# Kernel optimization log

Measured on AMD Instinct MI355X. Metric: run time of the kernel, lower is better.

Reference implementation:

```python
import jax, jax.numpy as jnp
from jax import lax
import numpy as np

N_PATTS, D_PATTS, L_PATTS = 64, 16, 64
L_OUT = L_PATTS  # module sets l_out = l_patts in both branches
RHO = 0.1
W = RHO ** (1.0 / L_PATTS)  # per-step decay weight
BIG = 1e30  # stands in for +inf at DP boundaries (avoids inf*0 nans)


def _dtw_matrix(x, patts, w):
    """Weighted-DTW DP matrix.
    x: (B, d, T), patts: (P, d, L) -> D: (B, P, L, T)
    D[i,j] = dist[i,j] + w * min(D[i-1,j], D[i,j-1], D[i-1,j-1]),
    with out-of-range predecessors = +inf and D[0,0] = dist[0,0].
    dist is the euclidean distance between x[:, :, j] and patts[:, :, i].
    """
    B, d, T = x.shape
    P, _, L = patts.shape
    x2 = jnp.sum(x * x, axis=1)              # (B, T)
    p2 = jnp.sum(patts * patts, axis=1)      # (P, L)
    xp = jnp.einsum('bdt,pdl->btpl', x, patts)  # (B, T, P, L)
    sq = x2[:, :, None, None] + p2[None, None, :, :] - 2.0 * xp
    dist = jnp.sqrt(jnp.maximum(sq, 1e-12))  # (B, T, P, L)
    dist_t = jnp.transpose(dist, (1, 0, 2, 3))  # (T, B, P, L) scan over time

    def col_step(prev_col, d_col):
        # prev_col = D[:, j-1] of shape (B, P, L); d_col = dist column (B, P, L)
        shifted = jnp.concatenate(
            [jnp.full_like(prev_col[..., :1], BIG), prev_col[..., :-1]], axis=-1)
        c = jnp.minimum(prev_col, shifted)  # min(D[i,j-1], D[i-1,j-1]) per i

        def cell(d_prev, inp):
            dist_i, c_i = inp              # each (B, P)
            m = jnp.minimum(d_prev, c_i)   # min over the 3 predecessors
            val = dist_i + jnp.where(m >= BIG * 0.5, 0.0, w * m)
            return val, val

        init = jnp.full(prev_col.shape[:2], BIG, prev_col.dtype)  # D[-1, j]
        _, col = lax.scan(
            cell, init,
            (jnp.moveaxis(d_col, -1, 0), jnp.moveaxis(c, -1, 0)))  # over i
        col = jnp.moveaxis(col, 0, -1)  # (B, P, L)
        return col, col

    init_col = jnp.full((B, P, L), BIG, dist.dtype)  # D[:, -1] = inf
    _, cols = lax.scan(col_step, init_col, dist_t)   # (T, B, P, L)
    return jnp.transpose(cols, (1, 2, 3, 0))         # (B, P, L, T)


def setup_inputs() -> dict:
    key = jax.random.key(0)
    kx, kp = jax.random.split(key)
    x = jax.random.normal(kx, (16, D_PATTS, 1024), dtype=jnp.float32)
    patts = jax.random.normal(kp, (N_PATTS, D_PATTS, L_PATTS), dtype=jnp.float32)
    return {"x": x, "patts": patts}


def reference(x, patts):
    D = _dtw_matrix(x, patts, W)          # (B, P, L, T)
    return D[:, :, :, -L_OUT:]            # last l_out time steps
```

## Files before the change

kernel.cpp:

```cpp
#include <hip/hip_runtime.h>
#include <math.h>

typedef _Float16 half8 __attribute__((ext_vector_type(8)));
typedef _Float16 h2 __attribute__((ext_vector_type(2)));
typedef float    f32x4 __attribute__((ext_vector_type(4)));
typedef unsigned int u32;
typedef unsigned long long u64;
typedef unsigned short u16;

#define BIGV 1e30f
#define RSTR 36

__device__ __forceinline__ u32 dpp_shr1(u32 oldv, u32 src) {
  return (u32)__builtin_amdgcn_update_dpp((int)oldv, (int)src, 0x138, 0xF, 0xF, false);
}
__device__ __forceinline__ float cvtlo(u32 v) {
  union { u16 u; _Float16 h; } c; c.u = (u16)v; return (float)c.h;
}
__device__ __forceinline__ u16 f2h(float f) {
  union { _Float16 h; u16 u; } c; c.h = (_Float16)f; return c.u;
}
__device__ __forceinline__ u32 pkrtz(float a, float b) {
  auto v = __builtin_amdgcn_cvt_pkrtz(a, b);
  union { decltype(v) h; u32 u; } c; c.h = v; return c.u;
}
__device__ __forceinline__ u32 funnel16(u32 hi, u32 lo, u32 sh) {
  return (u32)(((((u64)hi) << 32) | (u64)lo) >> sh);
}
__device__ __forceinline__ h2 as_h2(u32 u) { union { u32 u; h2 h; } x; x.u = u; return x.h; }

__global__ __launch_bounds__(256) void dtw_pc4(
    const float* __restrict__ x,
    const float* __restrict__ patts,
    float* __restrict__ out,
    float w) {
  __shared__ uint4 xsq[2050];
  __shared__ uint2 ring2[2 * 64 * RSTR];
  __shared__ u16   x2h16[1024];

  const int tid = threadIdx.x, lane = tid & 63, wv = tid >> 6;
  const int b = blockIdx.x >> 5, pg = blockIdx.x & 31;
  const int role = wv >> 1, pr = wv & 1;
  const int p = pg * 2 + pr;
  const int le = lane & 15, kq = lane >> 4;

  {
    const float* xb = x + b * (16 * 1024);
    u16* xh = (u16*)xsq;
    for (int idx = tid; idx < 16384; idx += 256) {
      int d = idx >> 10, t = idx & 1023;
      xh[t * 16 + d] = f2h(xb[idx]);
    }
    if (tid == 0) { xsq[2048] = make_uint4(0,0,0,0); xsq[2049] = make_uint4(0,0,0,0); }
    __syncthreads();
    for (int t = tid; t < 1024; t += 256) {
      uint4 a0 = xsq[2 * t], a1 = xsq[2 * t + 1];
      float s2 = __builtin_amdgcn_fdot2(as_h2(a0.x), as_h2(a0.x), 0.f, false);
      s2 = __builtin_amdgcn_fdot2(as_h2(a0.y), as_h2(a0.y), s2, false);
      s2 = __builtin_amdgcn_fdot2(as_h2(a0.z), as_h2(a0.z), s2, false);
      s2 = __builtin_amdgcn_fdot2(as_h2(a0.w), as_h2(a0.w), s2, false);
      s2 = __builtin_amdgcn_fdot2(as_h2(a1.x), as_h2(a1.x), s2, false);
      s2 = __builtin_amdgcn_fdot2(as_h2(a1.y), as_h2(a1.y), s2, false);
      s2 = __builtin_amdgcn_fdot2(as_h2(a1.z), as_h2(a1.z), s2, false);
      s2 = __builtin_amdgcn_fdot2(as_h2(a1.w), as_h2(a1.w), s2, false);
      x2h16[t] = f2h(s2);
    }
  }
  __syncthreads();

  if (role == 0) {
    half8 bf[4];
    {
      const float* pp = patts + p * (16 * 64);
#pragma unroll
      for (int nb = 0; nb < 4; ++nb) {
        float pv[8]; float part = 0.f;
#pragma unroll
        for (int j = 0; j < 8; ++j) {
          float f = (kq < 2) ? pp[(8 * kq + j) * 64 + nb * 16 + le] : 0.f;
          pv[j] = f; part = fmaf(f, f, part);
        }
        part += __shfl_xor(part, 16, 64);
        part += __shfl_xor(part, 32, 64);
        u32 wd0 = pkrtz(-2.f * pv[0], -2.f * pv[1]);
        u32 wd1 = pkrtz(-2.f * pv[2], -2.f * pv[3]);
        u32 wd2 = pkrtz(-2.f * pv[4], -2.f * pv[5]);
        u32 wd3 = pkrtz(-2.f * pv[6], -2.f * pv[7]);
        if (kq == 2) { wd0 = 0x3C00u | ((u32)f2h(part) << 16); wd1 = 0; wd2 = 0; wd3 = 0; }
        union { uint4 q; half8 h; } bu; bu.q = make_uint4(wd0, wd1, wd2, wd3);
        bf[nb] = bu.h;
      }
    }
    int colp = 8 * kq;
    const int wpbase = pr * (64 * RSTR) + RSTR * le;

#define PRODUCE(T0) { \
    int aidx_ = (kq < 2) ? (2 * ((T0) + le) + kq) : 2048; \
    uint4 aq_ = xsq[aidx_]; \
    u32 x2b_ = (u32)x2h16[(T0) + le]; \
    aq_.x = (kq == 2) ? (x2b_ | 0x3C000000u) : aq_.x; \
    union { uint4 q; half8 h; } au_; au_.q = aq_; \
    int wb_ = wpbase + (colp >> 3); \
    bool mir_ = colp < 32; \
    _Pragma("unroll") \
    for (int nb_ = 0; nb_ < 4; ++nb_) { \
      f32x4 c_ = {0.f, 0.f, 0.f, 0.f}; \
      c_ = __builtin_amdgcn_mfma_f32_16x16x32_f16(au_.h, bf[nb_], c_, 0, 0, 0); \
      float d0_ = __builtin_amdgcn_sqrtf(fmaxf(c_[0], 1e-12f)); \
      float d1_ = __builtin_amdgcn_sqrtf(fmaxf(c_[1], 1e-12f)); \
      float d2_ = __builtin_amdgcn_sqrtf(fmaxf(c_[2], 1e-12f)); \
      float d3_ = __builtin_amdgcn_sqrtf(fmaxf(c_[3], 1e-12f)); \
      uint2 st_; st_.x = pkrtz(d0_, d1_); st_.y = pkrtz(d2_, d3_); \
      ring2[wb_ + (16 * RSTR) * nb_] = st_; \
      if (mir_) ring2[wb_ + (16 * RSTR) * nb_ + 32] = st_; \
    } \
    colp = (colp + 32) & 255; }

    PRODUCE(0); PRODUCE(16); PRODUCE(32); PRODUCE(48);
    __syncthreads();
#pragma unroll 1
    for (int k = 0; k < 30; ++k) {
      PRODUCE(32 * k + 64);
      PRODUCE(32 * k + 80);
      __syncthreads();
    }
    __syncthreads(); __syncthreads(); __syncthreads(); __syncthreads();

  } else {
    const int rcbase = pr * (64 * RSTR) + RSTR * lane;
    int colc = (((0 - lane) >> 2) << 3) & 255;
    const int ph = (0 - lane) & 3;
    const u32 shv = (u32)((ph & 1) * 16);
    const bool sel2 = (ph & 2) != 0;
    float prev = BIGV, shA = BIGV, shB = BIGV, pend = 0.f;
    const int bigbits = __float_as_int(BIGV);
    float* oprow = out + ((b * 64 + p) * 64 + lane) * 64;

#define LOADQ(Q0,Q1,Q2,Q3,Q4) { int ci_ = rcbase + (colc >> 3); \
    Q0 = ring2[ci_];     Q1 = ring2[ci_ + 1]; Q2 = ring2[ci_ + 2]; \
    Q3 = ring2[ci_ + 3]; Q4 = ring2[ci_ + 4]; \
    colc = (colc + 32) & 255; }

#define SHIFT(curv) { shB = shA; \
    shA = __int_as_float((int)dpp_shr1((u32)bigbits, (u32)__float_as_int(curv))); \
    prev = (curv); }

#define STEP_PRO(S, D) { float dist_ = (D); \
    float m_ = fminf(fminf(prev, shA), shB); \
    float ms_ = (m_ >= 0.5e30f) ? 0.f : m_; \
    float val_ = fmaf(w, ms_, dist_); \
    int t_ = (S) - lane; float cur_ = (t_ >= 0) ? val_ : BIGV; \
    SHIFT(cur_); }

#define STEP_MAIN(S, D) { float dist_ = (D); \
    float m_ = fminf(fminf(prev, shA), shB); \
    float cur_ = fmaf(w, m_, dist_); \
    SHIFT(cur_); }

#define STEP_EPI(S, D) { float dist_ = (D); \
    float m_ = fminf(fminf(prev, shA), shB); \
    float val_ = fmaf(w, m_, dist_); \
    int t_ = (S) - lane; float cur_ = (t_ <= 1023) ? val_ : BIGV; \
    if ((t_ & 1) == 0) { pend = val_; } \
    else if ((u32)(t_ - 961) < 63u) { \
      *(float2*)(oprow + (t_ - 961)) = make_float2(pend, val_); } \
    SHIFT(cur_); }

#define EXTRACT8(Q0, Q1, Q2, Q3, Q4) \
    u32 W0_ = sel2 ? Q0.y : Q0.x, W1_ = sel2 ? Q1.x : Q0.y, \
        W2_ = sel2 ? Q1.y : Q1.x, W3_ = sel2 ? Q2.x : Q1.y, \
        W4_ = sel2 ? Q2.y : Q2.x, W5_ = sel2 ? Q3.x : Q2.y, \
        W6_ = sel2 ? Q3.y : Q3.x, W7_ = sel2 ? Q4.x : Q3.y, \
        W8_ = sel2 ? Q4.y : Q4.x; \
    u32 A0 = funnel16(W1_, W0_, shv), A1 = funnel16(W2_, W1_, shv), \
        A2 = funnel16(W3_, W2_, shv), A3 = funnel16(W4_, W3_, shv), \
        A4 = funnel16(W5_, W4_, shv), A5 = funnel16(W6_, W5_, shv), \
        A6 = funnel16(W7_, W6_, shv), A7 = funnel16(W8_, W7_, shv);

#define S16(S0, STP) \
    STP((S0)+0,  cvtlo(A0)); STP((S0)+1,  cvtlo(A0 >> 16)); \
    STP((S0)+2,  cvtlo(A1)); STP((S0)+3,  cvtlo(A1 >> 16)); \
    STP((S0)+4,  cvtlo(A2)); STP((S0)+5,  cvtlo(A2 >> 16)); \
    STP((S0)+6,  cvtlo(A3)); STP((S0)+7,  cvtlo(A3 >> 16)); \
    STP((S0)+8,  cvtlo(A4)); STP((S0)+9,  cvtlo(A4 >> 16)); \
    STP((S0)+10, cvtlo(A5)); STP((S0)+11, cvtlo(A5 >> 16)); \
    STP((S0)+12, cvtlo(A6)); STP((S0)+13, cvtlo(A6 >> 16)); \
    STP((S0)+14, cvtlo(A7)); STP((S0)+15, cvtlo(A7 >> 16));

#define SET_PRO(S0)  S16(S0, STEP_PRO)
#define SET_MAIN(S0) S16(S0, STEP_MAIN)
#define SET_EPI(S0)  S16(S0, STEP_EPI)

#define PHASE(C0,C1,C2,C3,C4,C5,C6,C7,C8,C9, L0,L1,L2,L3,L4,L5,L6,L7,L8,L9, S0, SETM) { \
    LOADQ(L0,L1,L2,L3,L4); LOADQ(L5,L6,L7,L8,L9); \
    { EXTRACT8(C0,C1,C2,C3,C4); SETM(S0); } \
    { EXTRACT8(C5,C6,C7,C8,C9); SETM((S0)+16); } \
    __syncthreads(); }

    __syncthreads();
    uint2 a0,a1,a2,a3,a4,a5,a6,a7,a8,a9;
    uint2 b0,b1,b2,b3,b4,b5,b6,b7,b8,b9;
    LOADQ(a0,a1,a2,a3,a4); LOADQ(a5,a6,a7,a8,a9);

    PHASE(a0,a1,a2,a3,a4,a5,a6,a7,a8,a9, b0,b1,b2,b3,b4,b5,b6,b7,b8,b9, 0,  SET_PRO);
    PHASE(b0,b1,b2,b3,b4,b5,b6,b7,b8,b9, a0,a1,a2,a3,a4,a5,a6,a7,a8,a9, 32, SET_PRO);
#pragma unroll 1
    for (int j = 1; j < 15; ++j) {
      PHASE(a0,a1,a2,a3,a4,a5,a6,a7,a8,a9, b0,b1,b2,b3,b4,b5,b6,b7,b8,b9, 64*j,      SET_MAIN);
      PHASE(b0,b1,b2,b3,b4,b5,b6,b7,b8,b9, a0,a1,a2,a3,a4,a5,a6,a7,a8,a9, 64*j + 32, SET_MAIN);
    }
    PHASE(a0,a1,a2,a3,a4,a5,a6,a7,a8,a9, b0,b1,b2,b3,b4,b5,b6,b7,b8,b9, 960,  SET_EPI);
    PHASE(b0,b1,b2,b3,b4,b5,b6,b7,b8,b9, a0,a1,a2,a3,a4,a5,a6,a7,a8,a9, 992,  SET_EPI);
    PHASE(a0,a1,a2,a3,a4,a5,a6,a7,a8,a9, b0,b1,b2,b3,b4,b5,b6,b7,b8,b9, 1024, SET_EPI);
    PHASE(b0,b1,b2,b3,b4,b5,b6,b7,b8,b9, a0,a1,a2,a3,a4,a5,a6,a7,a8,a9, 1056, SET_EPI);
  }
}

extern "C" void kernel_launch(void* const* d_in, const int* in_sizes, int n_in,
                              void* d_out, int out_size, void* d_ws, size_t ws_size,
                              hipStream_t stream) {
  const float* x     = (const float*)d_in[0];
  const float* patts = (const float*)d_in[1];
  float* out         = (float*)d_out;
  const float w = (float)exp(log(0.1) / 64.0);
  dim3 grid(512), block(256);
  hipLaunchKernelGGL(dtw_pc4, grid, block, 0, stream, x, patts, out, w);
}
```

Measured before the change: 51.57 us.

## Restructure into 768-thread blocks with 8 consumers and 4 dual-pattern producers

Changes the block from 2 producer plus 2 consumer waves for two patterns to 12 waves per block: 8 consumer waves handle 8 patterns and 4 producer waves each compute distances for two patterns. The grid shrinks from 512 to 128 blocks. The transposed fp16 x staging in shared memory is removed. Producers now read x straight from global memory and skew the tile per nb so that the ring row stride (37) avoids bank conflicts. The epilogue is split to drop one select, and raw s_barrier is used instead of __syncthreads. This trades fewer, larger blocks (which could leave many CUs idle) and repeated global loads of x against less staging work and fewer producer waves per pattern.

```diff
diff --git a/kernel.cpp b/kernel.cpp
--- a/kernel.cpp
+++ b/kernel.cpp
@@ -2,14 +2,14 @@
 #include <math.h>
 
 typedef _Float16 half8 __attribute__((ext_vector_type(8)));
-typedef _Float16 h2 __attribute__((ext_vector_type(2)));
 typedef float    f32x4 __attribute__((ext_vector_type(4)));
 typedef unsigned int u32;
 typedef unsigned long long u64;
 typedef unsigned short u16;
 
 #define BIGV 1e30f
-#define RSTR 36
+#define RQ 37
+#define PAIRQ (64 * RQ)
 
 __device__ __forceinline__ u32 dpp_shr1(u32 oldv, u32 src) {
   return (u32)__builtin_amdgcn_update_dpp((int)oldv, (int)src, 0x138, 0xF, 0xF, false);
@@ -27,58 +27,74 @@
 __device__ __forceinline__ u32 funnel16(u32 hi, u32 lo, u32 sh) {
   return (u32)(((((u64)hi) << 32) | (u64)lo) >> sh);
 }
-__device__ __forceinline__ h2 as_h2(u32 u) { union { u32 u; h2 h; } x; x.u = u; return x.h; }
-
-__global__ __launch_bounds__(256) void dtw_pc4(
+
+__global__ __launch_bounds__(768) void dtw_2c(
     const float* __restrict__ x,
     const float* __restrict__ patts,
     float* __restrict__ out,
-    float w) {
-  __shared__ uint4 xsq[2050];
-  __shared__ uint2 ring2[2 * 64 * RSTR];
+    float wd) {
+  __shared__ uint2 ring2[8 * PAIRQ];
   __shared__ u16   x2h16[1024];
 
   const int tid = threadIdx.x, lane = tid & 63, wv = tid >> 6;
-  const int b = blockIdx.x >> 5, pg = blockIdx.x & 31;
-  const int role = wv >> 1, pr = wv & 1;
-  const int p = pg * 2 + pr;
+  const int b = blockIdx.x >> 3, pg = blockIdx.x & 7;
   const int le = lane & 15, kq = lane >> 4;
-
-  {
-    const float* xb = x + b * (16 * 1024);
-    u16* xh = (u16*)xsq;
-    for (int idx = tid; idx < 16384; idx += 256) {
-      int d = idx >> 10, t = idx & 1023;
-      xh[t * 16 + d] = f2h(xb[idx]);
-    }
-    if (tid == 0) { xsq[2048] = make_uint4(0,0,0,0); xsq[2049] = make_uint4(0,0,0,0); }
-    __syncthreads();
-    for (int t = tid; t < 1024; t += 256) {
-      uint4 a0 = xsq[2 * t], a1 = xsq[2 * t + 1];
-      float s2 = __builtin_amdgcn_fdot2(as_h2(a0.x), as_h2(a0.x), 0.f, false);
-      s2 = __builtin_amdgcn_fdot2(as_h2(a0.y), as_h2(a0.y), s2, false);
-      s2 = __builtin_amdgcn_fdot2(as_h2(a0.z), as_h2(a0.z), s2, false);
-      s2 = __builtin_amdgcn_fdot2(as_h2(a0.w), as_h2(a0.w), s2, false);
-      s2 = __builtin_amdgcn_fdot2(as_h2(a1.x), as_h2(a1.x), s2, false);
-      s2 = __builtin_amdgcn_fdot2(as_h2(a1.y), as_h2(a1.y), s2, false);
-      s2 = __builtin_amdgcn_fdot2(as_h2(a1.z), as_h2(a1.z), s2, false);
-      s2 = __builtin_amdgcn_fdot2(as_h2(a1.w), as_h2(a1.w), s2, false);
-      x2h16[t] = f2h(s2);
-    }
+  const float* xb = x + b * (16 * 1024);
+
+  for (int t = tid; t < 1024; t += 768) {
+    float s2 = 0.f;
+#pragma unroll
+    for (int d = 0; d < 16; ++d) { float f = xb[d * 1024 + t]; s2 = fmaf(f, f, s2); }
+    x2h16[t] = f2h(s2);
   }
   __syncthreads();
 
-  if (role == 0) {
-    half8 bf[4];
-    {
-      const float* pp = patts + p * (16 * 64);
+#define PRODUCE(RB, BF, T0) { \
+    _Pragma("unroll") \
+    for (int nb_ = 0; nb_ < 4; ++nb_) { \
+      int t0n_ = (T0) - 16 * nb_; \
+      if ((u32)t0n_ < 1024u) { \
+        uint4 aq_; \
+        if (kq < 2) { \
+          const float* xp_ = xb + (8 * kq) * 1024 + t0n_ + le; \
+          aq_.x = pkrtz(xp_[0],    xp_[1024]); \
+          aq_.y = pkrtz(xp_[2048], xp_[3072]); \
+          aq_.z = pkrtz(xp_[4096], xp_[5120]); \
+          aq_.w = pkrtz(xp_[6144], xp_[7168]); \
+        } else if (kq == 2) { \
+          aq_ = make_uint4((u32)x2h16[t0n_ + le] | 0x3C000000u, 0u, 0u, 0u); \
+        } else { aq_ = make_uint4(0u, 0u, 0u, 0u); } \
+        union { uint4 q; half8 h; } au_; au_.q = aq_; \
+        f32x4 c_ = {0.f, 0.f, 0.f, 0.f}; \
+        c_ = __builtin_amdgcn_mfma_f32_16x16x32_f16(au_.h, (BF)[nb_], c_, 0, 0, 0); \
+        float d0_ = __builtin_amdgcn_sqrtf(fmaxf(c_[0], 1e-12f)); \
+        float d1_ = __builtin_amdgcn_sqrtf(fmaxf(c_[1], 1e-12f)); \
+        float d2_ = __builtin_amdgcn_sqrtf(fmaxf(c_[2], 1e-12f)); \
+        float d3_ = __builtin_amdgcn_sqrtf(fmaxf(c_[3], 1e-12f)); \
+        u32 coln_ = (u32)(((((T0) >> 4) - nb_) & 7) * 32 + 8 * kq); \
+        int wb_ = (RB) + 37 * le + 592 * nb_ + (int)(coln_ >> 3); \
+        uint2 st_; st_.x = pkrtz(d0_, d1_); st_.y = pkrtz(d2_, d3_); \
+        ring2[wb_] = st_; \
+        if (coln_ < 32u) ring2[wb_ + 32] = st_; \
+      } \
+    } }
+
+  if (wv >= 8) {
+    const int j = wv - 8;
+    const int prA = 2 * j, prB = 2 * j + 1;
+    const int rbA = prA * PAIRQ, rbB = prB * PAIRQ;
+    half8 bfA[4], bfB[4];
+#pragma unroll
+    for (int side = 0; side < 2; ++side) {
+      const float* pp = patts + (pg * 8 + (side ? prB : prA)) * (16 * 64);
+      half8* bf = side ? bfB : bfA;
 #pragma unroll
       for (int nb = 0; nb < 4; ++nb) {
         float pv[8]; float part = 0.f;
 #pragma unroll
-        for (int j = 0; j < 8; ++j) {
-          float f = (kq < 2) ? pp[(8 * kq + j) * 64 + nb * 16 + le] : 0.f;
-          pv[j] = f; part = fmaf(f, f, part);
+        for (int jj = 0; jj < 8; ++jj) {
+          float f = (kq < 2) ? pp[(8 * kq + jj) * 64 + nb * 16 + le] : 0.f;
+          pv[jj] = f; part = fmaf(f, f, part);
         }
         part += __shfl_xor(part, 16, 64);
         part += __shfl_xor(part, 32, 64);
@@ -91,43 +107,22 @@
         bf[nb] = bu.h;
       }
     }
-    int colp = 8 * kq;
-    const int wpbase = pr * (64 * RSTR) + RSTR * le;
-
-#define PRODUCE(T0) { \
-    int aidx_ = (kq < 2) ? (2 * ((T0) + le) + kq) : 2048; \
-    uint4 aq_ = xsq[aidx_]; \
-    u32 x2b_ = (u32)x2h16[(T0) + le]; \
-    aq_.x = (kq == 2) ? (x2b_ | 0x3C000000u) : aq_.x; \
-    union { uint4 q; half8 h; } au_; au_.q = aq_; \
-    int wb_ = wpbase + (colp >> 3); \
-    bool mir_ = colp < 32; \
-    _Pragma("unroll") \
-    for (int nb_ = 0; nb_ < 4; ++nb_) { \
-      f32x4 c_ = {0.f, 0.f, 0.f, 0.f}; \
-      c_ = __builtin_amdgcn_mfma_f32_16x16x32_f16(au_.h, bf[nb_], c_, 0, 0, 0); \
-      float d0_ = __builtin_amdgcn_sqrtf(fmaxf(c_[0], 1e-12f)); \
-      float d1_ = __builtin_amdgcn_sqrtf(fmaxf(c_[1], 1e-12f)); \
-      float d2_ = __builtin_amdgcn_sqrtf(fmaxf(c_[2], 1e-12f)); \
-      float d3_ = __builtin_amdgcn_sqrtf(fmaxf(c_[3], 1e-12f)); \
-      uint2 st_; st_.x = pkrtz(d0_, d1_); st_.y = pkrtz(d2_, d3_); \
-      ring2[wb_ + (16 * RSTR) * nb_] = st_; \
-      if (mir_) ring2[wb_ + (16 * RSTR) * nb_ + 32] = st_; \
-    } \
-    colp = (colp + 32) & 255; }
-
-    PRODUCE(0); PRODUCE(16); PRODUCE(32); PRODUCE(48);
+    PRODUCE(rbA, bfA, 0);  PRODUCE(rbA, bfA, 16); PRODUCE(rbA, bfA, 32); PRODUCE(rbA, bfA, 48);
+    PRODUCE(rbB, bfB, 0);  PRODUCE(rbB, bfB, 16); PRODUCE(rbB, bfB, 32); PRODUCE(rbB, bfB, 48);
     __syncthreads();
 #pragma unroll 1
-    for (int k = 0; k < 30; ++k) {
-      PRODUCE(32 * k + 64);
-      PRODUCE(32 * k + 80);
+    for (int k = 0; k < 34; ++k) {
+      if (k < 32) {
+        PRODUCE(rbA, bfA, 32 * k + 64); PRODUCE(rbA, bfA, 32 * k + 80);
+        PRODUCE(rbB, bfB, 32 * k + 64); PRODUCE(rbB, bfB, 32 * k + 80);
+      }
       __syncthreads();
     }
-    __syncthreads(); __syncthreads(); __syncthreads(); __syncthreads();
 
   } else {
-    const int rcbase = pr * (64 * RSTR) + RSTR * lane;
+    const int pr = wv;
+    const int p = pg * 8 + pr;
+    const int rcbase = pr * PAIRQ + RQ * lane;
     int colc = (((0 - lane) >> 2) << 3) & 255;
     const int ph = (0 - lane) & 3;
     const u32 shv = (u32)((ph & 1) * 16);
@@ -148,22 +143,31 @@
 #define STEP_PRO(S, D) { float dist_ = (D); \
     float m_ = fminf(fminf(prev, shA), shB); \
     float ms_ = (m_ >= 0.5e30f) ? 0.f : m_; \
-    float val_ = fmaf(w, ms_, dist_); \
+    float val_ = fmaf(wd, ms_, dist_); \
     int t_ = (S) - lane; float cur_ = (t_ >= 0) ? val_ : BIGV; \
     SHIFT(cur_); }
 
 #define STEP_MAIN(S, D) { float dist_ = (D); \
     float m_ = fminf(fminf(prev, shA), shB); \
-    float cur_ = fmaf(w, m_, dist_); \
+    float cur_ = fmaf(wd, m_, dist_); \
     SHIFT(cur_); }
 
-#define STEP_EPI(S, D) { float dist_ = (D); \
-    float m_ = fminf(fminf(prev, shA), shB); \
-    float val_ = fmaf(w, m_, dist_); \
+#define STEP_EPI2(S, D) { float dist_ = (D); \
+    float m_ = fminf(fminf(prev, shA), shB); \
+    float val_ = fmaf(wd, m_, dist_); \
+    int t_ = (S) - lane; \
+    if ((t_ & 1) == 0) { pend = val_; } \
+    else if ((u32)(t_ - 961) < 63u) \
+      *(float2*)(oprow + (t_ - 961)) = make_float2(pend, val_); \
+    SHIFT(val_); }
+
+#define STEP_EPI3(S, D) { float dist_ = (D); \
+    float m_ = fminf(fminf(prev, shA), shB); \
+    float val_ = fmaf(wd, m_, dist_); \
     int t_ = (S) - lane; float cur_ = (t_ <= 1023) ? val_ : BIGV; \
     if ((t_ & 1) == 0) { pend = val_; } \
-    else if ((u32)(t_ - 961) < 63u) { \
-      *(float2*)(oprow + (t_ - 961)) = make_float2(pend, val_); } \
+    else if ((u32)(t_ - 961) < 63u) \
+      *(float2*)(oprow + (t_ - 961)) = make_float2(pend, val_); \
     SHIFT(cur_); }
 
 #define EXTRACT8(Q0, Q1, Q2, Q3, Q4) \
@@ -189,15 +193,16 @@
 
 #define SET_PRO(S0)  S16(S0, STEP_PRO)
 #define SET_MAIN(S0) S16(S0, STEP_MAIN)
-#define SET_EPI(S0)  S16(S0, STEP_EPI)
+#define SET_EPI2(S0) S16(S0, STEP_EPI2)
+#define SET_EPI3(S0) S16(S0, STEP_EPI3)
 
 #define PHASE(C0,C1,C2,C3,C4,C5,C6,C7,C8,C9, L0,L1,L2,L3,L4,L5,L6,L7,L8,L9, S0, SETM) { \
     LOADQ(L0,L1,L2,L3,L4); LOADQ(L5,L6,L7,L8,L9); \
     { EXTRACT8(C0,C1,C2,C3,C4); SETM(S0); } \
     { EXTRACT8(C5,C6,C7,C8,C9); SETM((S0)+16); } \
-    __syncthreads(); }
-
-    __syncthreads();
+    __builtin_amdgcn_s_barrier(); }
+
+    __builtin_amdgcn_s_barrier();
     uint2 a0,a1,a2,a3,a4,a5,a6,a7,a8,a9;
     uint2 b0,b1,b2,b3,b4,b5,b6,b7,b8,b9;
     LOADQ(a0,a1,a2,a3,a4); LOADQ(a5,a6,a7,a8,a9);
@@ -209,10 +214,10 @@
       PHASE(a0,a1,a2,a3,a4,a5,a6,a7,a8,a9, b0,b1,b2,b3,b4,b5,b6,b7,b8,b9, 64*j,      SET_MAIN);
       PHASE(b0,b1,b2,b3,b4,b5,b6,b7,b8,b9, a0,a1,a2,a3,a4,a5,a6,a7,a8,a9, 64*j + 32, SET_MAIN);
     }
-    PHASE(a0,a1,a2,a3,a4,a5,a6,a7,a8,a9, b0,b1,b2,b3,b4,b5,b6,b7,b8,b9, 960,  SET_EPI);
-    PHASE(b0,b1,b2,b3,b4,b5,b6,b7,b8,b9, a0,a1,a2,a3,a4,a5,a6,a7,a8,a9, 992,  SET_EPI);
-    PHASE(a0,a1,a2,a3,a4,a5,a6,a7,a8,a9, b0,b1,b2,b3,b4,b5,b6,b7,b8,b9, 1024, SET_EPI);
-    PHASE(b0,b1,b2,b3,b4,b5,b6,b7,b8,b9, a0,a1,a2,a3,a4,a5,a6,a7,a8,a9, 1056, SET_EPI);
+    PHASE(a0,a1,a2,a3,a4,a5,a6,a7,a8,a9, b0,b1,b2,b3,b4,b5,b6,b7,b8,b9, 960,  SET_EPI2);
+    PHASE(b0,b1,b2,b3,b4,b5,b6,b7,b8,b9, a0,a1,a2,a3,a4,a5,a6,a7,a8,a9, 992,  SET_EPI2);
+    PHASE(a0,a1,a2,a3,a4,a5,a6,a7,a8,a9, b0,b1,b2,b3,b4,b5,b6,b7,b8,b9, 1024, SET_EPI3);
+    PHASE(b0,b1,b2,b3,b4,b5,b6,b7,b8,b9, a0,a1,a2,a3,a4,a5,a6,a7,a8,a9, 1056, SET_EPI3);
   }
 }
 
@@ -223,6 +228,6 @@
   const float* patts = (const float*)d_in[1];
   float* out         = (float*)d_out;
   const float w = (float)exp(log(0.1) / 64.0);
-  dim3 grid(512), block(256);
-  hipLaunchKernelGGL(dtw_pc4, grid, block, 0, stream, x, patts, out, w);
-}
+  dim3 grid(128), block(768);
+  hipLaunchKernelGGL(dtw_2c, grid, block, 0, stream, x, patts, out, w);
+}
```

After: 171.3 us. 3.32x slower.
